# Performance work log

Hardware: AMD Instinct MI355X
Metric: run time of the kernel (lower is better)

The kernel has to match this reference:

```python
import jax, jax.numpy as jnp
import numpy as np

N_NODES = 100000
N_EDGES = 1600000
FEAT = 512
CLS = 64
HID = 200  # each hop layer output width; 3 hops -> 600 concat


def spmm(row, col, vals, x):
    # out[r] = sum_{e: row[e]==r} vals[e] * x[col[e]]  -- sparse A @ x
    return jax.ops.segment_sum(x[col] * vals[:, None], row, num_segments=x.shape[0])


def setup_inputs() -> dict:
    key = jax.random.key(0)
    ks = jax.random.split(key, 12)
    adj_index = jax.random.randint(ks[0], (2, N_EDGES), 0, N_NODES, dtype=jnp.int64)
    # scale like a normalized adjacency (~1/avg_degree) to keep powers stable
    adj_values = jax.random.uniform(ks[1], (N_EDGES,), dtype=jnp.float32) * (1.0 / 16.0)
    features = jax.random.normal(ks[2], (N_NODES, FEAT), dtype=jnp.float32)
    s1 = (2.0 / (FEAT + HID)) ** 0.5
    s2 = (2.0 / (3 * HID + HID)) ** 0.5
    sf = (2.0 / (3 * HID + CLS)) ** 0.5
    W1 = jax.random.normal(ks[3], (3, FEAT, HID), dtype=jnp.float32) * s1
    b1 = jax.random.normal(ks[4], (3, HID), dtype=jnp.float32) * 0.01
    W2 = jax.random.normal(ks[5], (3, 3 * HID, HID), dtype=jnp.float32) * s2
    b2 = jax.random.normal(ks[6], (3, HID), dtype=jnp.float32) * 0.01
    Wfc = jax.random.normal(ks[7], (3 * HID, CLS), dtype=jnp.float32) * sf
    bfc = jax.random.normal(ks[8], (CLS,), dtype=jnp.float32) * 0.01
    return {"adj_index": adj_index, "adj_values": adj_values, "features": features,
            "W1": W1, "b1": b1, "W2": W2, "b2": b2, "Wfc": Wfc, "bfc": bfc}


def reference(adj_index, adj_values, features, W1, b1, W2, b2, Wfc, bfc):
    # Inference mode: dropout is identity.
    row, col = adj_index[0], adj_index[1]
    # upper (sparse) layers: linear + bias + relu, then (iterations-1) spmm hops
    outs1 = []
    for i in range(3):  # iterations = i + 1
        h = jax.nn.relu(features @ W1[i] + b1[i][None, :])
        for _ in range(i):
            h = spmm(row, col, adj_values, h)
        outs1.append(h)
    abstract1 = jnp.concatenate(outs1, axis=1)  # [N, 600]
    # bottom (dense) layers: linear, (iterations-1) spmm hops, then + bias
    outs2 = []
    for i in range(3):
        h = abstract1 @ W2[i]
        for _ in range(i):
            h = spmm(row, col, adj_values, h)
        h = h + b2[i][None, :]
        outs2.append(h)
    abstract2 = jnp.concatenate(outs2, axis=1)  # [N, 600]
    node_emb = abstract2 @ Wfc + bfc  # [N, CLS]
    predictions = jax.nn.log_softmax(node_emb, axis=1)
    return node_emb, predictions
```

## Files before the change

kernel.cpp:

```cpp
#include <hip/hip_runtime.h>

typedef unsigned short u16;
typedef unsigned int u32;
typedef __attribute__((ext_vector_type(8))) short short8;
typedef __attribute__((ext_vector_type(4))) float f32x4;
typedef __attribute__((ext_vector_type(4))) u32 u32x4;
typedef __attribute__((ext_vector_type(2))) u32 u32x2;

#define NN 100000
#define PAD 640

__device__ __forceinline__ float b2f(u16 u) {
    union { u32 i; float f; } v; v.i = ((u32)u) << 16; return v.f;
}
__device__ __forceinline__ u16 f2b(float f) {
    union { float f; u32 i; } v; v.f = f;
    u32 x = v.i;
    return (u16)((x + 0x7FFFu + ((x >> 16) & 1u)) >> 16);
}
__device__ __forceinline__ u32 pack2(float lo, float hi) {
    return (u32)f2b(lo) | ((u32)f2b(hi) << 16);
}
__device__ __forceinline__ float rdf(const void* p, size_t i, int f) {
    return f ? ((const float*)p)[i] : b2f(((const u16*)p)[i]);
}
__device__ __forceinline__ void gload16(const u16* g, u16* l) {
    __builtin_amdgcn_global_load_lds(
        (const __attribute__((address_space(1))) void*)g,
        (__attribute__((address_space(3))) void*)l, 16, 0, 0);
}

__global__ void probe_k(const int* __restrict__ idx,
                        const void* avals, const void* feats, const void* W1,
                        const void* b1, const void* W2, const void* b2,
                        const void* Wfc, const void* bfc,
                        int* __restrict__ flags) {
    if (blockIdx.x != 0 || threadIdx.x >= 64) return;
    int lane = threadIdx.x;
    int v0 = idx[2 * lane + 1];
    int v1 = idx[2 * (lane + 64) + 1];
    int ok = (v0 == 0 && v1 == 0);
    int allz = __all(ok);
    if (lane == 0) flags[0] = allz ? 1 : 0;
    const void* ts[8] = {avals, feats, W1, b1, W2, b2, Wfc, bfc};
    const int ns[8] = {256, 256, 256, 128, 256, 128, 256, 32};
    for (int t = 0; t < 8; ++t) {
        const u16* p = (const u16*)ts[t];
        int n = ns[t], bad = 0;
        for (int i = lane; i < n; i += 64) {
            int e = (p[2 * i] >> 7) & 0xFF;
            if (e >= 133) bad++;
        }
        for (int off = 32; off; off >>= 1) bad += __shfl_xor(bad, off, 64);
        if (lane == 0) flags[1 + t] = (bad * 8 >= n) ? 1 : 0;
    }
}

__device__ __forceinline__ int load_row(const int* idx, int E, int f, int e) {
    return f ? idx[2 * e] : idx[e];
}
__device__ __forceinline__ int load_col(const int* idx, int E, int f, int e) {
    return f ? idx[2 * E + 2 * e] : idx[E + e];
}

__global__ void prep_k(const void* __restrict__ W1, const void* __restrict__ W2,
                       const void* __restrict__ Wfc,
                       const void* __restrict__ b1, const void* __restrict__ b2,
                       const void* __restrict__ bfc,
                       u16* __restrict__ w1t, u16* __restrict__ w2t,
                       u16* __restrict__ wfct, float* __restrict__ biasf,
                       const int* __restrict__ flags) {
    int i = blockIdx.x * 256 + threadIdx.x;
    int job = blockIdx.y;
    if (job == 0) {
        if (i >= 640 * 512) return;
        int n = i >> 9, k = i & 511;
        float v = 0.f;
        if (n < 600) {
            int ib = n / 200, c = n % 200;
            v = rdf(W1, (size_t)ib * 102400 + (size_t)k * 200 + c, flags[3]);
        }
        w1t[i] = f2b(v);
    } else if (job == 1) {
        if (i >= 640 * 640) return;
        int n = i / 640, k = i % 640;
        float v = 0.f;
        if (n < 600 && k < 600) {
            int ib = n / 200, c = n % 200;
            v = rdf(W2, (size_t)ib * 120000 + (size_t)k * 200 + c, flags[5]);
        }
        w2t[i] = f2b(v);
    } else if (job == 2) {
        if (i >= 64 * 640) return;
        int n = i / 640, k = i % 640;
        float v = 0.f;
        if (k < 600) v = rdf(Wfc, (size_t)k * 64 + n, flags[7]);
        wfct[i] = f2b(v);
    } else if (job == 3) {
        if (i < 600) biasf[i] = rdf(b1, i, flags[4]);
        else if (i < 1200) biasf[i] = rdf(b2, i - 600, flags[6]);
        else if (i < 1264) biasf[i] = rdf(bfc, i - 1200, flags[8]);
    } else {
        if (i >= 64) return;
        int fb2 = flags[6], fwf = flags[7];
        float s = rdf(bfc, i, flags[8]);
        for (int k = 0; k < 200; ++k)
            s += rdf(b2, k, fb2) * rdf(Wfc, (size_t)k * 64 + i, fwf);
        biasf[1280 + i] = s;
    }
}

__device__ __forceinline__ int pad8(int c) { return (c + 7) & ~7; }

__global__ void count_k(const int* __restrict__ idx, int E, const int* __restrict__ flags,
                        int* __restrict__ counts) {
    int e = blockIdx.x * 256 + threadIdx.x;
    if (e >= E) return;
    int r = load_row(idx, E, flags[0], e);
    if ((u32)r >= NN) return;
    atomicAdd(&counts[r], 1);
}

__global__ void chunksum_k(const int* __restrict__ counts, int* __restrict__ chsum) {
    __shared__ int sm[256];
    int c = blockIdx.x, t = threadIdx.x;
    int base = c * 1024, s = 0;
    for (int i = t; i < 1024; i += 256) {
        int g = base + i;
        if (g < NN) s += pad8(counts[g]);
    }
    sm[t] = s; __syncthreads();
    for (int off = 128; off; off >>= 1) {
        if (t < off) sm[t] += sm[t + off];
        __syncthreads();
    }
    if (t == 0) chsum[c] = sm[0];
}

__global__ void chscan_k(const int* __restrict__ chsum, int nch, int* __restrict__ choff,
                         int* __restrict__ row_ptr, int E) {
    if (threadIdx.x == 0 && blockIdx.x == 0) {
        int run = 0;
        for (int c = 0; c < nch; ++c) { choff[c] = run; run += chsum[c]; }
        row_ptr[NN] = run;
    }
}

__global__ __launch_bounds__(1024) void scan_k(const int* __restrict__ counts,
                                               const int* __restrict__ choff,
                                               int* __restrict__ row_ptr,
                                               int* __restrict__ cursor) {
    __shared__ int sm[1024];
    int c = blockIdx.x, t = threadIdx.x;
    int g = c * 1024 + t;
    int v = (g < NN) ? pad8(counts[g]) : 0;
    sm[t] = v;
    __syncthreads();
    for (int off = 1; off < 1024; off <<= 1) {
        int add = (t >= off) ? sm[t - off] : 0;
        __syncthreads();
        sm[t] += add;
        __syncthreads();
    }
    if (g < NN) {
        int ex = choff[c] + sm[t] - v;
        row_ptr[g] = ex;
        cursor[g] = ex;
    }
}

__global__ void scatter_k(const int* __restrict__ idx, const void* __restrict__ avals, int E,
                          const int* __restrict__ flags, int* __restrict__ cursor,
                          int* __restrict__ edges) {
    int e = blockIdx.x * 256 + threadIdx.x;
    if (e >= E) return;
    int f = flags[0];
    int r = load_row(idx, E, f, e);
    if ((u32)r >= NN) return;
    int c = load_col(idx, E, f, e);
    if ((u32)c >= NN) c = 0;
    int p = atomicAdd(&cursor[r], 1);
    edges[2 * p] = c;
    ((float*)edges)[2 * p + 1] = rdf(avals, e, flags[1]);
}

__global__ void padfill_k(const int* __restrict__ cursor, const int* __restrict__ row_ptr,
                          int* __restrict__ edges) {
    int r = blockIdx.x * 256 + threadIdx.x;
    if (r >= NN) return;
    int p = cursor[r], e = row_ptr[r + 1];
    for (; p < e; ++p) {
        edges[2 * p] = 0;
        ((float*)edges)[2 * p + 1] = 0.f;
    }
}

__global__ __launch_bounds__(256) void gemm1_k(
    const void* __restrict__ A, const u16* __restrict__ Bt,
    u16* __restrict__ C, u16* __restrict__ Cc,
    const float* __restrict__ bias, const int* __restrict__ flags,
    int M, int K, int lda, int ldc) {
    __shared__ u16 As[128 * 32];
    __shared__ u16 Bs[128 * 32];
    const int tid = threadIdx.x;
    const int wave = tid >> 6, lane = tid & 63;

    const int nwg = gridDim.x;
    const int q = nwg >> 3, r8 = nwg & 7;
    const int xcd = blockIdx.x & 7, lo = blockIdx.x >> 3;
    const int wg = (xcd < r8 ? xcd * (q + 1) : r8 * (q + 1) + (xcd - r8) * q) + lo;
    const int bmi = wg / 5, bni = wg - bmi * 5;
    const int bm = bmi * 128, bn = bni * 128;

    const int wrow = (wave >> 1) * 64, wcol = (wave & 1) * 64;
    const int l15 = lane & 15, l4 = lane >> 4;
    f32x4 acc[4][4] = {};

    const int ff = flags[2];
    const int c0 = wave * 2;
    const int rowA0 = c0 * 16 + (lane >> 2);
    const int rowA1 = rowA0 + 16;
    const int colE = (lane & 3) * 8;
    int gr0 = bm + rowA0; if (gr0 >= M) gr0 = M - 1;
    int gr1 = bm + rowA1; if (gr1 >= M) gr1 = M - 1;
    const float* a0f = (const float*)A + (size_t)gr0 * lda + colE;
    const float* a1f = (const float*)A + (size_t)gr1 * lda + colE;
    const u16* a0h = (const u16*)A + (size_t)gr0 * lda + colE;
    const u16* a1h = (const u16*)A + (size_t)gr1 * lda + colE;
    const u16* b0p = Bt + (size_t)(bn + rowA0) * K + colE;
    const u16* b1p = Bt + (size_t)(bn + rowA1) * K + colE;
    u16* lA0 = &As[rowA0 * 32 + colE];
    u16* lA1 = &As[rowA1 * 32 + colE];
    u16* lB0 = Bs + c0 * 512;
    u16* lB1 = Bs + c0 * 512 + 512;

    for (int k0 = 0; k0 < K; k0 += 32) {
        short8 av0, av1;
        if (ff) {
            f32x4 x0 = *(const f32x4*)(a0f + k0);
            f32x4 x1 = *(const f32x4*)(a0f + k0 + 4);
            f32x4 y0 = *(const f32x4*)(a1f + k0);
            f32x4 y1 = *(const f32x4*)(a1f + k0 + 4);
#pragma unroll
            for (int t = 0; t < 4; ++t) {
                av0[t] = (short)f2b(x0[t]); av0[t + 4] = (short)f2b(x1[t]);
                av1[t] = (short)f2b(y0[t]); av1[t + 4] = (short)f2b(y1[t]);
            }
        } else {
            av0 = *(const short8*)(a0h + k0);
            av1 = *(const short8*)(a1h + k0);
        }
        __syncthreads();
        *(short8*)lA0 = av0;
        *(short8*)lA1 = av1;
        gload16(b0p + k0, lB0);
        gload16(b1p + k0, lB1);
        __syncthreads();
        short8 af[4], bf[4];
#pragma unroll
        for (int t = 0; t < 4; ++t) {
            af[t] = *(const short8*)&As[(wrow + t * 16 + l15) * 32 + l4 * 8];
            bf[t] = *(const short8*)&Bs[(wcol + t * 16 + l15) * 32 + l4 * 8];
        }
#pragma unroll
        for (int mi = 0; mi < 4; ++mi)
#pragma unroll
            for (int ni = 0; ni < 4; ++ni)
                acc[mi][ni] = __builtin_amdgcn_mfma_f32_16x16x32_bf16(
                    af[mi], bf[ni], acc[mi][ni], 0, 0, 0);
    }

#pragma unroll
    for (int mi = 0; mi < 4; ++mi)
#pragma unroll
        for (int ni = 0; ni < 4; ++ni)
#pragma unroll
            for (int r4 = 0; r4 < 4; ++r4) {
                int row = bm + wrow + mi * 16 + l4 * 4 + r4;
                int col = bn + wcol + ni * 16 + l15;
                if (row < M) {
                    float v = acc[mi][ni][r4];
                    if (col < 600) v += bias[col];
                    v = fmaxf(v, 0.0f);
                    u16 b = f2b(v);
                    C[(size_t)row * ldc + col] = b;
                    if (col < 200 || col >= 600)
                        Cc[(size_t)row * ldc + col] = b;
                }
            }
}

__global__ __launch_bounds__(256) void gemm128_k(
    const u16* __restrict__ A, const u16* __restrict__ Bt,
    u16* __restrict__ C, float* __restrict__ Cf,
    const float* __restrict__ bias, int bias_n, int relu,
    int M, int K, int lda, int ldc) {
    __shared__ u16 As[128 * 32];
    __shared__ u16 Bs[128 * 32];
    const int tid = threadIdx.x;
    const int wave = tid >> 6, lane = tid & 63;

    const int nwg = gridDim.x;
    const int q = nwg >> 3, r8 = nwg & 7;
    const int xcd = blockIdx.x & 7, lo = blockIdx.x >> 3;
    const int wg = (xcd < r8 ? xcd * (q + 1) : r8 * (q + 1) + (xcd - r8) * q) + lo;
    const int bmi = wg / 5, bni = wg - bmi * 5;
    const int bm = bmi * 128, bn = bni * 128;

    const int wrow = (wave >> 1) * 64, wcol = (wave & 1) * 64;
    const int l15 = lane & 15, l4 = lane >> 4;
    f32x4 acc[4][4] = {};

    const int c0 = wave * 2;
    const int rowA0 = c0 * 16 + (lane >> 2);
    const int rowA1 = rowA0 + 16;
    const int colE = (lane & 3) * 8;
    int gr0 = bm + rowA0; if (gr0 >= M) gr0 = M - 1;
    int gr1 = bm + rowA1; if (gr1 >= M) gr1 = M - 1;
    const u16* a0p = A + (size_t)gr0 * lda + colE;
    const u16* a1p = A + (size_t)gr1 * lda + colE;
    const u16* b0p = Bt + (size_t)(bn + rowA0) * K + colE;
    const u16* b1p = Bt + (size_t)(bn + rowA1) * K + colE;
    u16* lA0 = As + c0 * 512;
    u16* lA1 = As + c0 * 512 + 512;
    u16* lB0 = Bs + c0 * 512;
    u16* lB1 = Bs + c0 * 512 + 512;

    for (int k0 = 0; k0 < K; k0 += 32) {
        __syncthreads();
        gload16(a0p + k0, lA0);
        gload16(a1p + k0, lA1);
        gload16(b0p + k0, lB0);
        gload16(b1p + k0, lB1);
        __syncthreads();
        short8 af[4], bf[4];
#pragma unroll
        for (int t = 0; t < 4; ++t) {
            af[t] = *(const short8*)&As[(wrow + t * 16 + l15) * 32 + l4 * 8];
            bf[t] = *(const short8*)&Bs[(wcol + t * 16 + l15) * 32 + l4 * 8];
        }
#pragma unroll
        for (int mi = 0; mi < 4; ++mi)
#pragma unroll
            for (int ni = 0; ni < 4; ++ni)
                acc[mi][ni] = __builtin_amdgcn_mfma_f32_16x16x32_bf16(
                    af[mi], bf[ni], acc[mi][ni], 0, 0, 0);
    }

#pragma unroll
    for (int mi = 0; mi < 4; ++mi)
#pragma unroll
        for (int ni = 0; ni < 4; ++ni)
#pragma unroll
            for (int r4 = 0; r4 < 4; ++r4) {
                int row = bm + wrow + mi * 16 + l4 * 4 + r4;
                int col = bn + wcol + ni * 16 + l15;
                if (row < M) {
                    float v = acc[mi][ni][r4];
                    if (bias && col < bias_n) v += bias[col];
                    if (relu) v = fmaxf(v, 0.0f);
                    if (C) C[(size_t)row * ldc + col] = f2b(v);
                    if (Cf) Cf[(size_t)row * ldc + col] = v;
                }
            }
}

__global__ __launch_bounds__(256) void fc64_k(
    const u16* __restrict__ A0, const u16* __restrict__ A1,
    const u16* __restrict__ Bt,
    float* __restrict__ out_ne, float* __restrict__ out_pred,
    const float* __restrict__ bias, int M, int K, int lda) {
    __shared__ __align__(16) char ldsbuf[128 * 64 * 4];
    u16* As = (u16*)ldsbuf;
    u16* Bs = (u16*)(ldsbuf + 8192);
    float* smC = (float*)ldsbuf;

    const int tid = threadIdx.x;
    const int wave = tid >> 6, lane = tid & 63;
    const int bm = blockIdx.x * 128;
    const int wrow = (wave >> 1) * 64, wcol = (wave & 1) * 32;
    const int l15 = lane & 15, l4 = lane >> 4;
    f32x4 acc[4][2] = {};

    const int colE = (lane & 3) * 8;
    int gr0 = bm + wave * 32 + (lane >> 2); if (gr0 >= M) gr0 = M - 1;
    int gr1 = bm + wave * 32 + 16 + (lane >> 2); if (gr1 >= M) gr1 = M - 1;
    const u16* a0p0 = A0 + (size_t)gr0 * lda + colE;
    const u16* a0p1 = A1 + (size_t)gr0 * lda + colE;
    const u16* a1p0 = A0 + (size_t)gr1 * lda + colE;
    const u16* a1p1 = A1 + (size_t)gr1 * lda + colE;
    const u16* bp = Bt + (size_t)(wave * 16 + (lane >> 2)) * K + colE;
    u16* lA0 = As + wave * 1024;
    u16* lA1 = As + wave * 1024 + 512;
    u16* lB = Bs + wave * 512;

    for (int k0 = 0; k0 < K; k0 += 32) {
        const bool in0 = (k0 + colE) < 200;
        const u16* pa0 = in0 ? a0p0 : a0p1;
        const u16* pa1 = in0 ? a1p0 : a1p1;
        __syncthreads();
        gload16(pa0 + k0, lA0);
        gload16(pa1 + k0, lA1);
        gload16(bp + k0, lB);
        __syncthreads();
        short8 af[4], bf[2];
#pragma unroll
        for (int t = 0; t < 4; ++t)
            af[t] = *(const short8*)&As[(wrow + t * 16 + l15) * 32 + l4 * 8];
#pragma unroll
        for (int t = 0; t < 2; ++t)
            bf[t] = *(const short8*)&Bs[(wcol + t * 16 + l15) * 32 + l4 * 8];
#pragma unroll
        for (int mi = 0; mi < 4; ++mi)
#pragma unroll
            for (int ni = 0; ni < 2; ++ni)
                acc[mi][ni] = __builtin_amdgcn_mfma_f32_16x16x32_bf16(
                    af[mi], bf[ni], acc[mi][ni], 0, 0, 0);
    }

    __syncthreads();
#pragma unroll
    for (int mi = 0; mi < 4; ++mi)
#pragma unroll
        for (int ni = 0; ni < 2; ++ni)
#pragma unroll
            for (int r4 = 0; r4 < 4; ++r4) {
                int rl = wrow + mi * 16 + l4 * 4 + r4;
                int col = wcol + ni * 16 + l15;
                int row = bm + rl;
                float v = acc[mi][ni][r4] + bias[col];
                smC[rl * 64 + col] = v;
                if (row < M) out_ne[(size_t)row * 64 + col] = v;
            }
    __syncthreads();

    const int rl = tid >> 1, half = tid & 1;
    const int row = bm + rl;
    float vv[32];
#pragma unroll
    for (int k = 0; k < 32; ++k) {
        int c = half * 32 + ((k + rl) & 31);
        vv[k] = smC[rl * 64 + c];
    }
    float m = vv[0];
#pragma unroll
    for (int k = 1; k < 32; ++k) m = fmaxf(m, vv[k]);
    m = fmaxf(m, __shfl_xor(m, 1, 64));
    float s = 0.f;
#pragma unroll
    for (int k = 0; k < 32; ++k) s += expf(vv[k] - m);
    s += __shfl_xor(s, 1, 64);
    float lg = m + logf(s);
    if (row < M) {
#pragma unroll
        for (int k = 0; k < 32; ++k) {
            int c = half * 32 + ((k + rl) & 31);
            out_pred[(size_t)row * 64 + c] = vv[k] - lg;
        }
    }
}

__global__ __launch_bounds__(256) void spmm400_k(
    const int* __restrict__ row_ptr, const int* __restrict__ edges,
    const u16* __restrict__ X, u16* __restrict__ Y1, u16* __restrict__ Yt,
    const float* __restrict__ bias1) {
    int r = blockIdx.x * 4 + (threadIdx.x >> 6);
    if (r >= NN) return;
    int lane = threadIdx.x & 63;
    int s = row_ptr[r], e = row_ptr[r + 1];
    if (s < 0) s = 0;
    if (e < s) e = s;
    float a[8] = {0.f, 0.f, 0.f, 0.f, 0.f, 0.f, 0.f, 0.f};
    const bool act = lane < 50;
    const u32* xl = (const u32*)X + lane * 4;
    for (int i = s; i < e; i += 8) {
        int cc[8]; float vv[8];
#pragma unroll
        for (int j = 0; j < 4; ++j) {
            u32x4 p = *(const u32x4*)(edges + 2 * (size_t)(i + 2 * j));
            union { u32 u; float f; } w0, w1;
            cc[2 * j] = (int)p[0];     w0.u = p[1];
            cc[2 * j + 1] = (int)p[2]; w1.u = p[3];
            vv[2 * j] = w0.f; vv[2 * j + 1] = w1.f;
        }
        if (act) {
            u32x4 g[8];
#pragma unroll
            for (int j = 0; j < 8; ++j) {
                u32 c = (u32)cc[j]; if (c >= NN) c = 0;
                g[j] = *(const u32x4*)(xl + (size_t)c * 320);
            }
#pragma unroll
            for (int j = 0; j < 8; ++j) {
                float v = vv[j];
#pragma unroll
                for (int q = 0; q < 4; ++q) {
                    union { u32 i; float f; } lo, hi;
                    lo.i = g[j][q] << 16; hi.i = g[j][q] & 0xffff0000u;
                    a[2 * q] = fmaf(v, lo.f, a[2 * q]);
                    a[2 * q + 1] = fmaf(v, hi.f, a[2 * q + 1]);
                }
            }
        }
    }
    if (bias1 && lane < 25) {
#pragma unroll
        for (int q = 0; q < 8; ++q) a[q] += bias1[lane * 8 + q];
    }
    u32x4 o;
    o[0] = pack2(a[0], a[1]); o[1] = pack2(a[2], a[3]);
    o[2] = pack2(a[4], a[5]); o[3] = pack2(a[6], a[7]);
    if (lane < 25) {
        *(u32x4*)((u32*)Y1 + (size_t)r * 320 + lane * 4) = o;
    } else if (lane < 50) {
        *(u32x4*)((u32*)Yt + (size_t)r * 100 + (lane - 25) * 4) = o;
    }
}

__global__ __launch_bounds__(256) void spmm200_k(
    const int* __restrict__ row_ptr, const int* __restrict__ edges,
    const u16* __restrict__ X, int ldx,
    u16* __restrict__ Y, int ldy,
    const float* __restrict__ bias) {
    int r = blockIdx.x * 4 + (threadIdx.x >> 6);
    if (r >= NN) return;
    int lane = threadIdx.x & 63;
    int s = row_ptr[r], e = row_ptr[r + 1];
    if (s < 0) s = 0;
    if (e < s) e = s;
    float a[4] = {0.f, 0.f, 0.f, 0.f};
    const bool act = lane < 50;
    const int ldxw = ldx >> 1, ldyw = ldy >> 1;
    const u32* xl = (const u32*)X + lane * 2;
    for (int i = s; i < e; i += 8) {
        int cc[8]; float vv[8];
#pragma unroll
        for (int j = 0; j < 4; ++j) {
            u32x4 p = *(const u32x4*)(edges + 2 * (size_t)(i + 2 * j));
            union { u32 u; float f; } w0, w1;
            cc[2 * j] = (int)p[0];     w0.u = p[1];
            cc[2 * j + 1] = (int)p[2]; w1.u = p[3];
            vv[2 * j] = w0.f; vv[2 * j + 1] = w1.f;
        }
        if (act) {
            u32x2 g[8];
#pragma unroll
            for (int j = 0; j < 8; ++j) {
                u32 c = (u32)cc[j]; if (c >= NN) c = 0;
                g[j] = *(const u32x2*)(xl + (size_t)c * ldxw);
            }
#pragma unroll
            for (int j = 0; j < 8; ++j) {
                float v = vv[j];
#pragma unroll
                for (int q = 0; q < 2; ++q) {
                    union { u32 i; float f; } lo, hi;
                    lo.i = g[j][q] << 16; hi.i = g[j][q] & 0xffff0000u;
                    a[2 * q] = fmaf(v, lo.f, a[2 * q]);
                    a[2 * q + 1] = fmaf(v, hi.f, a[2 * q + 1]);
                }
            }
        }
    }
    if (bias && act) {
#pragma unroll
        for (int q = 0; q < 4; ++q) a[q] += bias[lane * 4 + q];
    }
    if (act) {
        u32x2 o;
        o[0] = pack2(a[0], a[1]); o[1] = pack2(a[2], a[3]);
        *(u32x2*)((u32*)Y + (size_t)r * ldyw + lane * 2) = o;
    }
}

extern "C" void kernel_launch(void* const* d_in, const int* in_sizes, int n_in,
                              void* d_out, int out_size, void* d_ws, size_t ws_size,
                              hipStream_t stream) {
    const int* adj_idx = (const int*)d_in[0];
    const void* adj_vals = d_in[1];
    const void* feats = d_in[2];
    const void* W1 = d_in[3];
    const void* b1 = d_in[4];
    const void* W2 = d_in[5];
    const void* b2 = d_in[6];
    const void* Wfc = d_in[7];
    const void* bfc = d_in[8];
    const int E = in_sizes[1];
    (void)n_in; (void)out_size; (void)ws_size;

    char* ws = (char*)d_ws;
    size_t off = 0;
    auto alloc = [&](size_t b) { size_t o = off; off += (b + 255) & ~(size_t)255; return o; };
    u16* buf0 = (u16*)(ws + alloc((size_t)NN * PAD * 2));
    u16* buf1 = (u16*)(ws + alloc((size_t)NN * PAD * 2));
    u16* hop = (u16*)(ws + alloc((size_t)NN * 200 * 2));
    u16* w1t = (u16*)(ws + alloc((size_t)640 * 512 * 2));
    u16* w2t = (u16*)(ws + alloc((size_t)640 * 640 * 2));
    u16* wfct = (u16*)(ws + alloc((size_t)64 * 640 * 2));
    float* biasf = (float*)(ws + alloc(1344 * 4));
    int* counts = (int*)(ws + alloc((size_t)NN * 4));
    int* cursor = (int*)(ws + alloc((size_t)NN * 4));
    int* row_ptr = (int*)(ws + alloc((size_t)(NN + 1) * 4));
    int* chsum = (int*)(ws + alloc(4096));
    int* choff = (int*)(ws + alloc(4096));
    int* flags = (int*)(ws + alloc(256));
    int* edgesS = (int*)(ws + alloc(((size_t)E + 8 * (size_t)NN) * 8));

    float* out_ne = (float*)d_out;
    float* out_pred = out_ne + (size_t)NN * 64;

    probe_k<<<1, 64, 0, stream>>>(adj_idx, adj_vals, feats, W1, b1, W2, b2, Wfc, bfc, flags);
    dim3 gp(1600, 5);
    prep_k<<<gp, 256, 0, stream>>>(W1, W2, Wfc, b1, b2, bfc, w1t, w2t, wfct, biasf, flags);

    hipMemsetAsync(counts, 0, NN * 4, stream);
    count_k<<<(E + 255) / 256, 256, 0, stream>>>(adj_idx, E, flags, counts);
    const int NCH = (NN + 1023) / 1024;
    chunksum_k<<<NCH, 256, 0, stream>>>(counts, chsum);
    chscan_k<<<1, 64, 0, stream>>>(chsum, NCH, choff, row_ptr, E);
    scan_k<<<NCH, 1024, 0, stream>>>(counts, choff, row_ptr, cursor);
    scatter_k<<<(E + 255) / 256, 256, 0, stream>>>(adj_idx, adj_vals, E, flags, cursor, edgesS);
    padfill_k<<<(NN + 255) / 256, 256, 0, stream>>>(cursor, row_ptr, edgesS);

    const int NWG = ((NN + 127) / 128) * 5;
    gemm1_k<<<NWG, 256, 0, stream>>>(feats, w1t, buf0, buf1, biasf, flags, NN, 512, 512, PAD);
    spmm400_k<<<(NN + 3) / 4, 256, 0, stream>>>(row_ptr, edgesS,
                                                buf0 + 200, buf1 + 200, hop, nullptr);
    spmm200_k<<<(NN + 3) / 4, 256, 0, stream>>>(row_ptr, edgesS,
                                                hop, 200, buf1 + 400, PAD, nullptr);
    gemm128_k<<<NWG, 256, 0, stream>>>(buf1, w2t, buf0, nullptr, nullptr, 0, 0, NN, PAD, PAD, PAD);
    spmm400_k<<<(NN + 3) / 4, 256, 0, stream>>>(row_ptr, edgesS,
                                                buf0 + 200, buf1 + 200, hop, biasf + 800);
    spmm200_k<<<(NN + 3) / 4, 256, 0, stream>>>(row_ptr, edgesS,
                                                hop, 200, buf1 + 400, PAD, biasf + 1000);
    fc64_k<<<(NN + 127) / 128, 256, 0, stream>>>(buf0, buf1, wfct, out_ne, out_pred,
                                                 biasf + 1280, NN, PAD, PAD);
}
```

Before: 1.521 ms.

## Double-buffer LDS tiles in gemm1 and prefetch A two steps ahead

The first GEMM kernel now keeps two LDS buffers for A and B. Each iteration stages the next B tile with direct global-to-LDS loads, writes the already-loaded next A tile, and issues global loads for the tile after that, all before running the MFMAs on the current buffer. This cuts the two barriers per K-step to one and overlaps global memory latency with compute. In exchange it doubles LDS use, which may lower occupancy, and keeps extra prefetch registers live.

```diff
diff --git a/kernel.cpp b/kernel.cpp
--- a/kernel.cpp
+++ b/kernel.cpp
@@ -200,8 +200,8 @@
     u16* __restrict__ C, u16* __restrict__ Cc,
     const float* __restrict__ bias, const int* __restrict__ flags,
     int M, int K, int lda, int ldc) {
-    __shared__ u16 As[128 * 32];
-    __shared__ u16 Bs[128 * 32];
+    __shared__ u16 As[2][128 * 32];
+    __shared__ u16 Bs[2][128 * 32];
     const int tid = threadIdx.x;
     const int wave = tid >> 6, lane = tid & 63;
 
@@ -229,38 +229,57 @@
     const u16* a1h = (const u16*)A + (size_t)gr1 * lda + colE;
     const u16* b0p = Bt + (size_t)(bn + rowA0) * K + colE;
     const u16* b1p = Bt + (size_t)(bn + rowA1) * K + colE;
-    u16* lA0 = &As[rowA0 * 32 + colE];
-    u16* lA1 = &As[rowA1 * 32 + colE];
-    u16* lB0 = Bs + c0 * 512;
-    u16* lB1 = Bs + c0 * 512 + 512;
-
-    for (int k0 = 0; k0 < K; k0 += 32) {
-        short8 av0, av1;
+    const int aoff0 = rowA0 * 32 + colE;
+    const int aoff1 = rowA1 * 32 + colE;
+
+    f32x4 x0a, x1a, x0b, x1b;
+    short8 h0, h1;
+
+    auto loadA = [&](int k0) {
         if (ff) {
-            f32x4 x0 = *(const f32x4*)(a0f + k0);
-            f32x4 x1 = *(const f32x4*)(a0f + k0 + 4);
-            f32x4 y0 = *(const f32x4*)(a1f + k0);
-            f32x4 y1 = *(const f32x4*)(a1f + k0 + 4);
+            x0a = *(const f32x4*)(a0f + k0); x1a = *(const f32x4*)(a0f + k0 + 4);
+            x0b = *(const f32x4*)(a1f + k0); x1b = *(const f32x4*)(a1f + k0 + 4);
+        } else {
+            h0 = *(const short8*)(a0h + k0);
+            h1 = *(const short8*)(a1h + k0);
+        }
+    };
+    auto writeA = [&](int buf) {
+        short8 w0, w1;
+        if (ff) {
 #pragma unroll
             for (int t = 0; t < 4; ++t) {
-                av0[t] = (short)f2b(x0[t]); av0[t + 4] = (short)f2b(x1[t]);
-                av1[t] = (short)f2b(y0[t]); av1[t + 4] = (short)f2b(y1[t]);
-            }
-        } else {
-            av0 = *(const short8*)(a0h + k0);
-            av1 = *(const short8*)(a1h + k0);
-        }
-        __syncthreads();
-        *(short8*)lA0 = av0;
-        *(short8*)lA1 = av1;
-        gload16(b0p + k0, lB0);
-        gload16(b1p + k0, lB1);
-        __syncthreads();
+                w0[t] = (short)f2b(x0a[t]); w0[t + 4] = (short)f2b(x1a[t]);
+                w1[t] = (short)f2b(x0b[t]); w1[t + 4] = (short)f2b(x1b[t]);
+            }
+        } else { w0 = h0; w1 = h1; }
+        *(short8*)&As[buf][aoff0] = w0;
+        *(short8*)&As[buf][aoff1] = w1;
+    };
+    auto stageB = [&](int buf, int k0) {
+        gload16(b0p + k0, &Bs[buf][c0 * 512]);
+        gload16(b1p + k0, &Bs[buf][c0 * 512 + 512]);
+    };
+
+    const int NT = K >> 5;
+    loadA(0);
+    writeA(0);
+    stageB(0, 0);
+    loadA(32);
+    __syncthreads();
+
+    int cur = 0;
+    for (int t = 0; t < NT; ++t) {
+        if (t + 1 < NT) {
+            stageB(cur ^ 1, (t + 1) << 5);
+            writeA(cur ^ 1);
+            if (t + 2 < NT) loadA((t + 2) << 5);
+        }
         short8 af[4], bf[4];
 #pragma unroll
-        for (int t = 0; t < 4; ++t) {
-            af[t] = *(const short8*)&As[(wrow + t * 16 + l15) * 32 + l4 * 8];
-            bf[t] = *(const short8*)&Bs[(wcol + t * 16 + l15) * 32 + l4 * 8];
+        for (int tt = 0; tt < 4; ++tt) {
+            af[tt] = *(const short8*)&As[cur][(wrow + tt * 16 + l15) * 32 + l4 * 8];
+            bf[tt] = *(const short8*)&Bs[cur][(wcol + tt * 16 + l15) * 32 + l4 * 8];
         }
 #pragma unroll
         for (int mi = 0; mi < 4; ++mi)
@@ -268,6 +287,8 @@
             for (int ni = 0; ni < 4; ++ni)
                 acc[mi][ni] = __builtin_amdgcn_mfma_f32_16x16x32_bf16(
                     af[mi], bf[ni], acc[mi][ni], 0, 0, 0);
+        __syncthreads();
+        cur ^= 1;
     }
 
 #pragma unroll
```

After: 1.521 ms. No clear change (-0.0%).
